# Kernel tuning notes

Measured on AMD Instinct MI355X. Metric: run time of the kernel, lower is better.

The kernel has to match this reference:

```python
import jax, jax.numpy as jnp
import numpy as np

B, T, D, H = 4, 2048, 512, 8
DH = D // H
SCALE = DH ** -0.5
CAUSAL = True


def setup_inputs() -> dict:
    key = jax.random.key(0)
    k1, k2, k3, k4 = jax.random.split(key, 4)
    x = jax.random.normal(k1, (B, T, D), dtype=jnp.float32)
    # realistic padding mask: each batch element has a random valid length
    lengths = jax.random.randint(k4, (B,), T // 2, T + 1)
    m = (jnp.arange(T)[None, :] < lengths[:, None]).astype(jnp.float32)[:, :, None]  # (B,T,1)
    w_qkv = jax.random.normal(k2, (D, 3 * D), dtype=jnp.float32) * (D ** -0.5)
    w_out = jax.random.normal(k3, (D, D), dtype=jnp.float32) * (D ** -0.5)
    b_out = jnp.zeros((D,), dtype=jnp.float32)
    return {"x": x, "m": m, "w_qkv": w_qkv, "w_out": w_out, "b_out": b_out}


def reference(x, m, w_qkv, w_out, b_out):
    qkv = x @ w_qkv
    q, k, v = jnp.split(qkv, 3, axis=-1)
    q = q.reshape(B, T, H, DH)
    k = k.reshape(B, T, H, DH)
    v = v.reshape(B, T, H, DH)
    # scores: (b,i,j,h), materialized like the torch module
    e = jnp.einsum('bihd,bjhd->bijh', q, k) * SCALE
    # key-padding mask (b,i,j)
    kpm = m[:, :, None, 0] * m[:, None, :, 0]
    if CAUSAL:
        kpm = jnp.tril(kpm)
    neg = -jnp.finfo(e.dtype).max
    e = jnp.where(kpm[..., None] == 0, neg, e)
    a = jax.nn.softmax(e, axis=2)
    o = jnp.einsum('bijh,bjhd->bihd', a, v).reshape(B, T, D)
    o = o @ w_out + b_out
    return o * m
```

## Files before the change

kernel.cpp:

```cpp
#include <hip/hip_runtime.h>
#include <hip/hip_bf16.h>

#define B_   4
#define T_   2048
#define D_   512
#define H_   8
#define DH_  64
#define BT_  (B_*T_)
#define N3D_ (3*D_)

typedef __bf16  bf16x8 __attribute__((ext_vector_type(8)));
typedef float   f32x4  __attribute__((ext_vector_type(4)));
typedef short   short8 __attribute__((ext_vector_type(8)));
typedef unsigned short u16;

#if defined(__has_builtin)
#if __has_builtin(__builtin_amdgcn_exp2f)
#define EXP2_OK 1
#endif
#endif
#ifndef EXP2_OK
#define EXP2_OK 0
#endif

#if EXP2_OK
#define QSCALE_F (0.125f * 1.44269504088896340736f)
static __device__ __forceinline__ float fastexp(float x) { return __builtin_amdgcn_exp2f(x); }
#else
#define QSCALE_F (0.125f)
static __device__ __forceinline__ float fastexp(float x) { return __expf(x); }
#endif

static __device__ __forceinline__ f32x4 fzero() { f32x4 z = {0.f,0.f,0.f,0.f}; return z; }

static __device__ __forceinline__ f32x4 mfma16(short8 a, short8 b, f32x4 c) {
  return __builtin_amdgcn_mfma_f32_16x16x32_bf16(
      __builtin_bit_cast(bf16x8, a), __builtin_bit_cast(bf16x8, b), c, 0, 0, 0);
}

static __device__ __forceinline__ int swz(int byteoff) {
  return byteoff ^ (((byteoff >> 7) & 7) << 4);
}

static __device__ __forceinline__ u16 bf16bits(float f) {
  __hip_bfloat16 h = __float2bfloat16(f);
  return *reinterpret_cast<u16*>(&h);
}

static __device__ __forceinline__ void gld_lds16(const void* g, void* l) {
  __builtin_amdgcn_global_load_lds(
      (const __attribute__((address_space(1))) void*)g,
      (__attribute__((address_space(3))) void*)l, 16, 0, 0);
}

#define XBLKS 768
__global__ __launch_bounds__(256) void prep_kernel(
    const float* __restrict__ x, const float* __restrict__ wqkv,
    const float* __restrict__ wout,
    u16* __restrict__ xb, u16* __restrict__ wqkvT, u16* __restrict__ woutT) {
  __shared__ u16 lt[64 * 72];
  const int tid = threadIdx.x;
  const int blk = blockIdx.x;

  if (blk < XBLKS) {
    const float4* x4 = reinterpret_cast<const float4*>(x);
    for (int idx = blk * 256 + tid; idx < BT_*D_/8; idx += XBLKS * 256) {
      float4 a = x4[idx*2], b = x4[idx*2+1];
      short8 o;
      o[0] = (short)bf16bits(a.x); o[1] = (short)bf16bits(a.y);
      o[2] = (short)bf16bits(a.z); o[3] = (short)bf16bits(a.w);
      o[4] = (short)bf16bits(b.x); o[5] = (short)bf16bits(b.y);
      o[6] = (short)bf16bits(b.z); o[7] = (short)bf16bits(b.w);
      *reinterpret_cast<short8*>(&xb[idx*8]) = o;
    }
    return;
  }

  int wb = blk - XBLKS;
  const float* src;
  u16* dst;
  int srcld, k0, n0;
  if (wb < 192) {
    src = wqkv; dst = wqkvT; srcld = N3D_;
    k0 = (wb & 7) * 64; n0 = (wb >> 3) * 64;
  } else {
    wb -= 192;
    src = wout; dst = woutT; srcld = D_;
    k0 = (wb & 7) * 64; n0 = (wb >> 3) * 64;
  }
  {
    int c = tid & 63, r0 = tid >> 6;
#pragma unroll
    for (int i = 0; i < 16; ++i) {
      int r = r0 * 16 + i;
      lt[r * 72 + c] = bf16bits(src[(long)(k0 + r) * srcld + n0 + c]);
    }
  }
  __syncthreads();
  {
    int kc = (tid & 7) * 8;
#pragma unroll
    for (int half = 0; half < 2; ++half) {
      int n = (tid >> 3) + half * 32;
      short8 v;
#pragma unroll
      for (int j = 0; j < 8; ++j) v[j] = (short)lt[(kc + j) * 72 + n];
      *reinterpret_cast<short8*>(&dst[(long)(n0 + n) * D_ + k0 + kc]) = v;
    }
  }
}

template <int MODE>
__global__ __launch_bounds__(256) void gemm_kernel(
    const u16* __restrict__ A, const u16* __restrict__ Wt,
    u16* __restrict__ qbuf, u16* __restrict__ kbuf, u16* __restrict__ vtbuf,
    const float* __restrict__ bias, const float* __restrict__ msk,
    float* __restrict__ out) {
  const int bn = blockIdx.x, bm = blockIdx.y;
  const int tid = threadIdx.x;
  const int w = tid >> 6, l = tid & 63;
  const int wr = w >> 1, wc = w & 1;
  const int lr = l & 15, lg = l >> 4;
  const int srow = l >> 3;
  const int scol = ((l & 7) ^ srow) << 4;

  __shared__ char ls[32768];
  char* lsA = ls;
  char* lsB = ls + 16384;

  f32x4 acc[4][4];
#pragma unroll
  for (int i = 0; i < 4; ++i)
#pragma unroll
    for (int j = 0; j < 4; ++j) acc[i][j] = fzero();

  const char* Ab = reinterpret_cast<const char*>(A) + (long)bm * 128 * 1024;
  const char* Wb = reinterpret_cast<const char*>(Wt) + (long)bn * 128 * 1024;

  for (int kt = 0; kt < 8; ++kt) {
#pragma unroll
    for (int c = 0; c < 4; ++c) {
      int chunk = w * 4 + c;
      int row = chunk * 8 + srow;
      gld_lds16(Ab + (long)row * 1024 + kt * 128 + scol, lsA + chunk * 1024);
      gld_lds16(Wb + (long)row * 1024 + kt * 128 + scol, lsB + chunk * 1024);
    }
    __syncthreads();

#pragma unroll
    for (int c = 0; c < 2; ++c) {
      short8 af[4], bfr[4];
#pragma unroll
      for (int mi = 0; mi < 4; ++mi) {
        int row = wr * 64 + mi * 16 + lr;
        af[mi] = *reinterpret_cast<const short8*>(
            lsA + swz(row * 128 + c * 64 + lg * 16));
      }
#pragma unroll
      for (int ni = 0; ni < 4; ++ni) {
        int row = wc * 64 + ni * 16 + lr;
        bfr[ni] = *reinterpret_cast<const short8*>(
            lsB + swz(row * 128 + c * 64 + lg * 16));
      }
      __builtin_amdgcn_s_setprio(1);
#pragma unroll
      for (int mi = 0; mi < 4; ++mi)
#pragma unroll
        for (int ni = 0; ni < 4; ++ni)
          acc[mi][ni] = mfma16(af[mi], bfr[ni], acc[mi][ni]);
      __builtin_amdgcn_s_setprio(0);
    }
    __syncthreads();
  }

  if (MODE == 0) {
    const int which = bn >> 2;
    if (which == 2) {
#pragma unroll
      for (int mi = 0; mi < 4; ++mi)
#pragma unroll
        for (int r = 0; r < 4; ++r) {
          int trow = wr * 64 + mi * 16 + lg * 4 + r;
#pragma unroll
          for (int ni = 0; ni < 4; ++ni) {
            int dcol = wc * 64 + ni * 16 + lr;
            int off = dcol * 256 + trow * 2;
            off ^= ((off >> 8) & 7) << 4;
            *reinterpret_cast<u16*>(ls + off) = bf16bits(acc[mi][ni][r]);
          }
        }
    } else {
      const float scale = (which == 0) ? QSCALE_F : 1.0f;
#pragma unroll
      for (int mi = 0; mi < 4; ++mi)
#pragma unroll
        for (int r = 0; r < 4; ++r) {
          int trow = wr * 64 + mi * 16 + lg * 4 + r;
#pragma unroll
          for (int ni = 0; ni < 4; ++ni) {
            int dcol = wc * 64 + ni * 16 + lr;
            int off = trow * 256 + dcol * 2;
            off ^= ((off >> 8) & 7) << 4;
            *reinterpret_cast<u16*>(ls + off) = bf16bits(acc[mi][ni][r] * scale);
          }
        }
    }
    __syncthreads();
    const int b = bm >> 4;
    const int tb0 = (bm & 15) * 128;
    if (which == 2) {
      const int bn8 = bn - 8;
#pragma unroll
      for (int it = 0; it < 8; ++it) {
        int dp = it * 16 + (tid >> 4);
        int tc = (tid & 15) * 16;
        int off = dp * 256 + (tc ^ ((dp & 7) << 4));
        short8 v = *reinterpret_cast<const short8*>(ls + off);
        int h = 2 * bn8 + (dp >> 6), d = dp & 63;
        long dst = ((long)((b * H_ + h) * DH_ + d)) * T_ + tb0 + tc / 2;
        *reinterpret_cast<short8*>(vtbuf + dst) = v;
      }
    } else {
      u16* obuf = (which == 0) ? qbuf : kbuf;
#pragma unroll
      for (int it = 0; it < 8; ++it) {
        int trow = it * 16 + (tid >> 4);
        int tc = (tid & 15) * 16;
        int off = trow * 256 + (tc ^ ((trow & 7) << 4));
        short8 v = *reinterpret_cast<const short8*>(ls + off);
        int dcol = tc / 2;
        int h = (bn & 3) * 2 + (dcol >> 6), d = dcol & 63;
        long dst = ((long)(b * H_ + h) * T_ + tb0 + trow) * DH_ + d;
        *reinterpret_cast<short8*>(obuf + dst) = v;
      }
    }
  } else {
#pragma unroll
    for (int mi = 0; mi < 4; ++mi) {
#pragma unroll
      for (int r = 0; r < 4; ++r) {
        int grow = bm * 128 + wr * 64 + mi * 16 + lg * 4 + r;
#pragma unroll
        for (int ni = 0; ni < 4; ++ni) {
          int gcol = bn * 128 + wc * 64 + ni * 16 + lr;
          float o = (acc[mi][ni][r] + bias[gcol]) * msk[grow];
          out[(long)grow * D_ + gcol] = o;
        }
      }
    }
  }
}

__global__ __launch_bounds__(512) void attn_kernel(
    const u16* __restrict__ q, const u16* __restrict__ k,
    const u16* __restrict__ vt, const float* __restrict__ msk,
    u16* __restrict__ ao) {
  const int bh = blockIdx.x;
  const int qt = 31 - blockIdx.y;
  const int b = bh >> 3, h = bh & 7;
  const int tid = threadIdx.x;
  const int w = tid >> 6;
  const int wq = w & 3;
  const int hf = w >> 2;
  const int l = tid & 63;
  const int lr = l & 15, lg = l >> 4;

  const float* mrow = msk + b * T_;

  unsigned long long bal = __ballot((l < 32) ? (mrow[l * 64] != 0.f) : false);
  const int nvalid = __popcll(bal);
  if (qt >= nvalid) return;
  const int nkv = (qt + 1 < nvalid) ? (qt + 1) : nvalid;
  const int nh = (nkv - hf + 1) >> 1;
  const int niter = (nkv + 1) >> 1;

  __shared__ char lsK[2 * 2 * 64 * 128];
  __shared__ char lsV[2 * 2 * 64 * 128];
  __shared__ char lsP[8 * 16 * 128];
  char* pbase = lsP + w * (16 * 128);
  char* myK = lsK + hf * 16384;
  char* myV = lsV + hf * 16384;

  const char* kb = reinterpret_cast<const char*>(k)  + (long)bh * T_ * 128;
  const char* vb = reinterpret_cast<const char*>(vt) + (long)bh * DH_ * T_ * 2;
  const char* qb = reinterpret_cast<const char*>(q);

  const int qrow0 = qt * 64 + wq * 16;

  short8 qf[2];
#pragma unroll
  for (int c = 0; c < 2; ++c)
    qf[c] = *reinterpret_cast<const short8*>(
        qb + (((long)bh * T_ + qrow0 + lr) * DH_ + c * 32 + lg * 8) * 2);

  const int srow = l >> 3;
  const int scol = ((l & 7) ^ srow) << 4;

  auto issue = [&](int kt_, int buf) {
#pragma unroll
    for (int c = 0; c < 2; ++c) {
      int chunk = wq * 2 + c;
      int row = chunk * 8 + srow;
      gld_lds16(kb + ((long)kt_ * 64 + row) * 128 + scol,
                myK + buf * 8192 + chunk * 1024);
      gld_lds16(vb + (long)row * (T_ * 2) + kt_ * 128 + scol,
                myV + buf * 8192 + chunk * 1024);
    }
  };

  if (0 < nh) issue(hf, 0);

  float mrun = -__builtin_inff(), lrun = 0.f;
  f32x4 oacc[4];
#pragma unroll
  for (int g = 0; g < 4; ++g) oacc[g] = fzero();

  for (int i = 0; i < niter; ++i) {
    __syncthreads();
    if (i + 1 < nh) issue(2 * (i + 1) + hf, (i + 1) & 1);
    if (i < nh) {
      const int kt = 2 * i + hf;
      const char* lk = myK + (i & 1) * 8192;
      const char* lv = myV + (i & 1) * 8192;

      f32x4 st[4];
      __builtin_amdgcn_s_setprio(1);
#pragma unroll
      for (int ni = 0; ni < 4; ++ni) {
        short8 kf0 = *reinterpret_cast<const short8*>(
            lk + swz((ni * 16 + lr) * 128 + lg * 16));
        short8 kf1 = *reinterpret_cast<const short8*>(
            lk + swz((ni * 16 + lr) * 128 + 64 + lg * 16));
        f32x4 z = fzero();
        z = mfma16(kf0, qf[0], z);
        z = mfma16(kf1, qf[1], z);
        st[ni] = z;
      }
      __builtin_amdgcn_s_setprio(0);

      const bool diag = (kt == qt);
      const bool needcm = (mrow[kt * 64 + 63] == 0.f);
      if (diag || needcm) {
#pragma unroll
        for (int ni = 0; ni < 4; ++ni)
#pragma unroll
          for (int r = 0; r < 4; ++r) {
            int jin = ni * 16 + lg * 4 + r;
            bool bad = (diag && jin > wq * 16 + lr) ||
                       (needcm && mrow[kt * 64 + jin] == 0.f);
            if (bad) st[ni][r] = -3.402823466e38f;
          }
      }

      float pmax = -3.402823466e38f;
#pragma unroll
      for (int ni = 0; ni < 4; ++ni)
#pragma unroll
        for (int r = 0; r < 4; ++r) pmax = fmaxf(pmax, st[ni][r]);
      pmax = fmaxf(pmax, __shfl_xor(pmax, 16));
      pmax = fmaxf(pmax, __shfl_xor(pmax, 32));

      if (!__all(pmax - mrun <= 8.f)) {
        float newm = fmaxf(mrun, pmax);
        float alpha = fastexp(mrun - newm);
        lrun *= alpha;
        mrun = newm;
#pragma unroll
        for (int rr = 0; rr < 4; ++rr) {
          float a = __shfl(alpha, lg * 4 + rr, 16);
#pragma unroll
          for (int g = 0; g < 4; ++g) oacc[g][rr] *= a;
        }
      }

      float p[4][4];
      float rs = 0.f;
#pragma unroll
      for (int ni = 0; ni < 4; ++ni)
#pragma unroll
        for (int r = 0; r < 4; ++r) {
          float pv = fastexp(st[ni][r] - mrun);
          p[ni][r] = pv;
          rs += pv;
        }
      rs += __shfl_xor(rs, 16);
      rs += __shfl_xor(rs, 32);
      lrun += rs;

#pragma unroll
      for (int ni = 0; ni < 4; ++ni)
#pragma unroll
        for (int rp = 0; rp < 2; ++rp) {
          unsigned lo = bf16bits(p[ni][2 * rp]);
          unsigned hi = bf16bits(p[ni][2 * rp + 1]);
          *reinterpret_cast<unsigned*>(
              pbase + swz(lr * 128 + ni * 32 + lg * 8 + rp * 4)) = lo | (hi << 16);
        }
      asm volatile("s_waitcnt lgkmcnt(0)" ::: "memory");

      __builtin_amdgcn_s_setprio(1);
#pragma unroll
      for (int c = 0; c < 2; ++c) {
        short8 pa = *reinterpret_cast<const short8*>(
            pbase + swz(lr * 128 + c * 64 + lg * 16));
#pragma unroll
        for (int g = 0; g < 4; ++g) {
          short8 vf = *reinterpret_cast<const short8*>(
              lv + swz((g * 16 + lr) * 128 + c * 64 + lg * 16));
          oacc[g] = mfma16(pa, vf, oacc[g]);
        }
      }
      __builtin_amdgcn_s_setprio(0);
    }
  }

  __syncthreads();
  float* mO  = reinterpret_cast<float*>(lsK);
  float* mML = reinterpret_cast<float*>(lsK + 4 * 4096);
  if (hf == 1) {
#pragma unroll
    for (int g = 0; g < 4; ++g)
#pragma unroll
      for (int rr = 0; rr < 4; ++rr)
        mO[wq * 1024 + (lg * 4 + rr) * 64 + g * 16 + lr] = oacc[g][rr];
    if (lg == 0) {
      mML[wq * 32 + lr * 2]     = mrun;
      mML[wq * 32 + lr * 2 + 1] = lrun;
    }
  }
  __syncthreads();
  if (hf == 0) {
    float m1 = mML[wq * 32 + lr * 2];
    float l1 = mML[wq * 32 + lr * 2 + 1];
    float M  = fmaxf(mrun, m1);
    float a0 = fastexp(mrun - M);
    float a1 = fastexp(m1 - M);
    float L  = a0 * lrun + a1 * l1;
#pragma unroll
    for (int rr = 0; rr < 4; ++rr) {
      int qrow = lg * 4 + rr;
      float a0r = __shfl(a0, qrow, 16);
      float a1r = __shfl(a1, qrow, 16);
      float Lr  = __shfl(L,  qrow, 16);
      float inv = 1.0f / Lr;
      int t = qrow0 + qrow;
#pragma unroll
      for (int g = 0; g < 4; ++g) {
        float o = a0r * oacc[g][rr] +
                  a1r * mO[wq * 1024 + qrow * 64 + g * 16 + lr];
        ao[((long)(b * T_ + t)) * D_ + h * 64 + g * 16 + lr] = bf16bits(o * inv);
      }
    }
  }
}

extern "C" void kernel_launch(void* const* d_in, const int* in_sizes, int n_in,
                              void* d_out, int out_size, void* d_ws,
                              size_t ws_size, hipStream_t stream) {
  const float* x    = (const float*)d_in[0];
  const float* msk  = (const float*)d_in[1];
  const float* wqkv = (const float*)d_in[2];
  const float* wout = (const float*)d_in[3];
  const float* bout = (const float*)d_in[4];
  float* out = (float*)d_out;

  char* ws = (char*)d_ws;
  u16* xb    = (u16*)(ws);
  u16* wqkvT = (u16*)(ws + 8388608);
  u16* woutT = (u16*)(ws + 9961472);
  u16* qbuf  = (u16*)(ws + 10485760);
  u16* kbuf  = (u16*)(ws + 18874368);
  u16* vtbuf = (u16*)(ws + 27262976);
  u16* ao    = (u16*)(ws + 35651584);

  prep_kernel<<<1024, 256, 0, stream>>>(x, wqkv, wout, xb, wqkvT, woutT);
  gemm_kernel<0><<<dim3(N3D_ / 128, BT_ / 128), 256, 0, stream>>>(
      xb, wqkvT, qbuf, kbuf, vtbuf, nullptr, nullptr, nullptr);
  attn_kernel<<<dim3(B_ * H_, T_ / 64), 512, 0, stream>>>(
      qbuf, kbuf, vtbuf, msk, ao);
  gemm_kernel<1><<<dim3(D_ / 128, BT_ / 128), 256, 0, stream>>>(
      ao, woutT, nullptr, nullptr, nullptr, bout, msk, out);
}
```

Before: 82.61 us.

## Double-buffer GEMM LDS tiles and remap blocks across XCDs

The projection GEMMs now prefetch the next K tile into a second LDS buffer while MFMAs run on the current one, with a single waitcnt plus barrier per iteration instead of two syncthreads. The grid becomes one-dimensional and block IDs are remapped so that consecutive tiles land on the same XCD, which is meant to improve L2 reuse of A rows. LDS use doubles to 64KB per block, which may lower occupancy. The GEMMs are a small part of total time next to attention.

```diff
diff --git a/kernel.cpp b/kernel.cpp
--- a/kernel.cpp
+++ b/kernel.cpp
@@ -116,7 +116,12 @@
     u16* __restrict__ qbuf, u16* __restrict__ kbuf, u16* __restrict__ vtbuf,
     const float* __restrict__ bias, const float* __restrict__ msk,
     float* __restrict__ out) {
-  const int bn = blockIdx.x, bm = blockIdx.y;
+  const int NBN = (MODE == 0) ? 12 : 4;
+  const int lin = blockIdx.x;
+  const int cpx = gridDim.x >> 3;
+  const int nn = (lin & 7) * cpx + (lin >> 3);
+  const int bm = nn / NBN, bn = nn % NBN;
+
   const int tid = threadIdx.x;
   const int w = tid >> 6, l = tid & 63;
   const int wr = w >> 1, wc = w & 1;
@@ -124,9 +129,7 @@
   const int srow = l >> 3;
   const int scol = ((l & 7) ^ srow) << 4;
 
-  __shared__ char ls[32768];
-  char* lsA = ls;
-  char* lsB = ls + 16384;
+  __shared__ char ls[2][32768];
 
   f32x4 acc[4][4];
 #pragma unroll
@@ -137,15 +140,25 @@
   const char* Ab = reinterpret_cast<const char*>(A) + (long)bm * 128 * 1024;
   const char* Wb = reinterpret_cast<const char*>(Wt) + (long)bn * 128 * 1024;
 
-  for (int kt = 0; kt < 8; ++kt) {
+  auto stage = [&](int kt, char* dst) {
 #pragma unroll
     for (int c = 0; c < 4; ++c) {
       int chunk = w * 4 + c;
       int row = chunk * 8 + srow;
-      gld_lds16(Ab + (long)row * 1024 + kt * 128 + scol, lsA + chunk * 1024);
-      gld_lds16(Wb + (long)row * 1024 + kt * 128 + scol, lsB + chunk * 1024);
-    }
-    __syncthreads();
+      gld_lds16(Ab + (long)row * 1024 + kt * 128 + scol, dst + chunk * 1024);
+      gld_lds16(Wb + (long)row * 1024 + kt * 128 + scol, dst + 16384 + chunk * 1024);
+    }
+  };
+
+  stage(0, ls[0]);
+  asm volatile("s_waitcnt vmcnt(0)" ::: "memory");
+  __builtin_amdgcn_s_barrier();
+
+  int cur = 0;
+  for (int kt = 0; kt < 8; ++kt) {
+    if (kt + 1 < 8) stage(kt + 1, ls[cur ^ 1]);
+    const char* lsA = ls[cur];
+    const char* lsB = ls[cur] + 16384;
 
 #pragma unroll
     for (int c = 0; c < 2; ++c) {
@@ -170,10 +183,14 @@
           acc[mi][ni] = mfma16(af[mi], bfr[ni], acc[mi][ni]);
       __builtin_amdgcn_s_setprio(0);
     }
-    __syncthreads();
+
+    asm volatile("s_waitcnt vmcnt(0)" ::: "memory");
+    __builtin_amdgcn_s_barrier();
+    cur ^= 1;
   }
 
   if (MODE == 0) {
+    char* lse = ls[0];
     const int which = bn >> 2;
     if (which == 2) {
 #pragma unroll
@@ -186,7 +203,7 @@
             int dcol = wc * 64 + ni * 16 + lr;
             int off = dcol * 256 + trow * 2;
             off ^= ((off >> 8) & 7) << 4;
-            *reinterpret_cast<u16*>(ls + off) = bf16bits(acc[mi][ni][r]);
+            *reinterpret_cast<u16*>(lse + off) = bf16bits(acc[mi][ni][r]);
           }
         }
     } else {
@@ -201,7 +218,7 @@
             int dcol = wc * 64 + ni * 16 + lr;
             int off = trow * 256 + dcol * 2;
             off ^= ((off >> 8) & 7) << 4;
-            *reinterpret_cast<u16*>(ls + off) = bf16bits(acc[mi][ni][r] * scale);
+            *reinterpret_cast<u16*>(lse + off) = bf16bits(acc[mi][ni][r] * scale);
           }
         }
     }
@@ -215,7 +232,7 @@
         int dp = it * 16 + (tid >> 4);
         int tc = (tid & 15) * 16;
         int off = dp * 256 + (tc ^ ((dp & 7) << 4));
-        short8 v = *reinterpret_cast<const short8*>(ls + off);
+        short8 v = *reinterpret_cast<const short8*>(lse + off);
         int h = 2 * bn8 + (dp >> 6), d = dp & 63;
         long dst = ((long)((b * H_ + h) * DH_ + d)) * T_ + tb0 + tc / 2;
         *reinterpret_cast<short8*>(vtbuf + dst) = v;
@@ -227,7 +244,7 @@
         int trow = it * 16 + (tid >> 4);
         int tc = (tid & 15) * 16;
         int off = trow * 256 + (tc ^ ((trow & 7) << 4));
-        short8 v = *reinterpret_cast<const short8*>(ls + off);
+        short8 v = *reinterpret_cast<const short8*>(lse + off);
         int dcol = tc / 2;
         int h = (bn & 3) * 2 + (dcol >> 6), d = dcol & 63;
         long dst = ((long)(b * H_ + h) * T_ + tb0 + trow) * DH_ + d;
@@ -474,10 +491,10 @@
   u16* ao    = (u16*)(ws + 35651584);
 
   prep_kernel<<<1024, 256, 0, stream>>>(x, wqkv, wout, xb, wqkvT, woutT);
-  gemm_kernel<0><<<dim3(N3D_ / 128, BT_ / 128), 256, 0, stream>>>(
+  gemm_kernel<0><<<(N3D_ / 128) * (BT_ / 128), 256, 0, stream>>>(
       xb, wqkvT, qbuf, kbuf, vtbuf, nullptr, nullptr, nullptr);
   attn_kernel<<<dim3(B_ * H_, T_ / 64), 512, 0, stream>>>(
       qbuf, kbuf, vtbuf, msk, ao);
-  gemm_kernel<1><<<dim3(D_ / 128, BT_ / 128), 256, 0, stream>>>(
+  gemm_kernel<1><<<(D_ / 128) * (BT_ / 128), 256, 0, stream>>>(
       ao, woutT, nullptr, nullptr, nullptr, bout, msk, out);
 }
```

New measurement: 70.77 us (median of 2 runs). -14.3%, faster.
